# Performance work log

Measured on AMD Instinct MI355X. Metric: run time of the kernel, lower is better.

The kernel has to match this reference:

```python
import jax, jax.numpy as jnp
import numpy as np

DIM = 128
HEADS = 4
DIM_HEAD = 32
HIDDEN = HEADS * DIM_HEAD  # 128
SCALE = DIM_HEAD ** -0.5


def setup_inputs() -> dict:
    key = jax.random.key(0)
    k1, k2, k3, k4 = jax.random.split(key, 4)
    b, c, h, w = 2, DIM, 64, 64
    x = jax.random.normal(k1, (b, c, h, w), dtype=jnp.float32)
    # conv1x1 weights stored as [out_ch, in_ch] (kernel is 1x1)
    w_qkv = jax.random.normal(k2, (3 * HIDDEN, DIM), dtype=jnp.float32) * (DIM ** -0.5)
    w_out = jax.random.normal(k3, (DIM, HIDDEN), dtype=jnp.float32) * (HIDDEN ** -0.5)
    b_out = jax.random.normal(k4, (DIM,), dtype=jnp.float32) * 0.01
    return {"x": x, "w_qkv": w_qkv, "w_out": w_out, "b_out": b_out}


def reference(x, w_qkv, w_out, b_out):
    b, c, h, w = x.shape
    n = h * w
    xf = x.reshape(b, c, n)                                   # [b,c,n]
    qkv = jnp.einsum('oc,bcn->bon', w_qkv, xf)                # conv1x1, no bias
    q, k, v = jnp.split(qkv, 3, axis=1)                       # each [b,hidden,n]
    q = q.reshape(b, HEADS, DIM_HEAD, n) * SCALE
    k = k.reshape(b, HEADS, DIM_HEAD, n)
    v = v.reshape(b, HEADS, DIM_HEAD, n)
    sim = jnp.einsum('bhdi,bhdj->bhij', q, k)                 # [b,h,n,n]
    attn = jax.nn.softmax(sim, axis=-1)
    out = jnp.einsum('bhij,bhdj->bhdi', attn, v)              # [b,h,d,n]
    out = out.reshape(b, HIDDEN, n)
    out = jnp.einsum('oc,bcn->bon', w_out, out) + b_out[None, :, None]
    return out.reshape(b, c, h, w) + x
```

## Files before the change

kernel.cpp:

```cpp
#include <hip/hip_runtime.h>
#include <hip/hip_bf16.h>

typedef __hip_bfloat16 bf16;
typedef float    f32x16 __attribute__((ext_vector_type(16)));
typedef __bf16   bf16x8 __attribute__((ext_vector_type(8)));
typedef unsigned uint4v __attribute__((ext_vector_type(4)));
typedef int      i32x2  __attribute__((ext_vector_type(2)));

#define N_TOK 4096
#define SCALE_L2E 0.2550348952703927f

__device__ __forceinline__ bf16x8 ld8(const bf16* p) { return *(const bf16x8*)p; }
__device__ __forceinline__ unsigned pack2(float a, float b) {
    unsigned short ua = __builtin_bit_cast(unsigned short, (__bf16)a);
    unsigned short ub = __builtin_bit_cast(unsigned short, (__bf16)b);
    return (unsigned)ua | ((unsigned)ub << 16);
}
__device__ __forceinline__ unsigned short f2b(float f) {
    return __builtin_bit_cast(unsigned short, (__bf16)f);
}
__device__ __forceinline__ __bf16 us2bf(unsigned short u) {
    return __builtin_bit_cast(__bf16, u);
}
__device__ __forceinline__ bf16x8 ldw(const unsigned short* rowp) {
    uint2 lo = *(const uint2*)rowp;
    uint2 hi = *(const uint2*)(rowp + 4);
    uint4v u = {lo.x, lo.y, hi.x, hi.y};
    return __builtin_bit_cast(bf16x8, u);
}

__global__ void __launch_bounds__(256)
qkv_mfma(const float* __restrict__ x, const float* __restrict__ w,
         bf16* __restrict__ qt, bf16* __restrict__ kt, bf16* __restrict__ vt) {
    int tok0 = blockIdx.x * 32;
    int b    = blockIdx.y;
    int z    = blockIdx.z;
    __shared__ unsigned short xs[128][32];
    __shared__ unsigned short wl[128][132];
    {
        int c = threadIdx.x >> 1, hf = threadIdx.x & 1;
        const float4* x4 = (const float4*)(x + (size_t)b * (128 * N_TOK) +
                                           (size_t)c * N_TOK + tok0 + hf * 16);
        float4 a = x4[0], bb = x4[1], cc = x4[2], dd = x4[3];
        unsigned* dst = (unsigned*)&xs[c][hf * 16];
        dst[0] = pack2(a.x, a.y);   dst[1] = pack2(a.z, a.w);
        dst[2] = pack2(bb.x, bb.y); dst[3] = pack2(bb.z, bb.w);
        dst[4] = pack2(cc.x, cc.y); dst[5] = pack2(cc.z, cc.w);
        dst[6] = pack2(dd.x, dd.y); dst[7] = pack2(dd.z, dd.w);
    }
    {
        float sc = (z == 0) ? SCALE_L2E : 1.0f;
        const float4* wb4 = (const float4*)(w + (size_t)z * 128 * 128);
#pragma unroll
        for (int s = 0; s < 16; ++s) {
            int i4 = threadIdx.x + s * 256;
            int o  = i4 >> 5, c4 = (i4 & 31) * 4;
            float4 wv4 = wb4[i4];
            *(uint2*)&wl[o][c4] = make_uint2(pack2(wv4.x * sc, wv4.y * sc),
                                             pack2(wv4.z * sc, wv4.w * sc));
        }
    }
    __syncthreads();
    int lane = threadIdx.x & 63, wv = threadIdx.x >> 6;
    int i = lane & 31, hl = lane >> 5;

    bf16x8 xf[8], wf[8];
#pragma unroll
    for (int kb = 0; kb < 8; ++kb) {
        bf16x8 f;
#pragma unroll
        for (int e = 0; e < 8; ++e) f[e] = us2bf(xs[kb * 16 + hl * 8 + e][i]);
        xf[kb] = f;
        wf[kb] = ldw(&wl[wv * 32 + i][kb * 16 + hl * 8]);
    }

    f32x16 D;
#pragma unroll
    for (int r = 0; r < 16; ++r) D[r] = 0.f;

    if (z < 2) {
#pragma unroll
        for (int kb = 0; kb < 8; ++kb)
            D = __builtin_amdgcn_mfma_f32_32x32x16_bf16(xf[kb], wf[kb], D, 0, 0, 0);
        bf16* base = (z == 0) ? qt : kt;
        unsigned short* dst = (unsigned short*)(base + ((size_t)(b * 4 + wv) * N_TOK + tok0) * 32);
#pragma unroll
        for (int r = 0; r < 16; ++r) {
            int tr = (r & 3) + 8 * (r >> 2) + 4 * hl;
            dst[tr * 32 + i] = f2b(D[r]);
        }
    } else {
#pragma unroll
        for (int kb = 0; kb < 8; ++kb)
            D = __builtin_amdgcn_mfma_f32_32x32x16_bf16(wf[kb], xf[kb], D, 0, 0, 0);
        unsigned short* dst = (unsigned short*)(vt + (size_t)(b * 4 + wv) * (32 * N_TOK) + tok0);
#pragma unroll
        for (int r = 0; r < 16; ++r) {
            int dr = (r & 3) + 8 * (r >> 2) + 4 * hl;
            dst[(size_t)dr * N_TOK + i] = f2b(D[r]);
        }
    }
}

__global__ void __launch_bounds__(512)
attn_mfma(const bf16* __restrict__ qt, const bf16* __restrict__ kt,
          const bf16* __restrict__ vt, bf16* __restrict__ ao) {
    int bid   = blockIdx.x;
    int swz   = (bid & 7) * 128 + (bid >> 3);
    int bh    = swz >> 7;
    int qtile = swz & 127;
    int lane  = threadIdx.x & 63;
    int wv    = threadIdx.x >> 6;
    int i     = lane & 31;
    int hl    = lane >> 5;

    const bf16* qb = qt + (size_t)bh * (N_TOK * 32) + (size_t)(qtile * 32) * 32;
    const bf16* kp0 = kt + (size_t)bh * (N_TOK * 32) + ((size_t)(wv * 512) + i) * 32 + hl * 8;
    const bf16* vp0 = vt + (size_t)bh * (32 * N_TOK) + (size_t)i * N_TOK + wv * 512 + hl * 8;

    bf16x8 q1 = ld8(qb + i * 32 + hl * 8);
    bf16x8 q2 = ld8(qb + i * 32 + 16 + hl * 8);

    bf16x8 ones;
#pragma unroll
    for (int e = 0; e < 8; ++e) ones[e] = us2bf(0x3F80);

    f32x16 O, Ol, Z;
#pragma unroll
    for (int r = 0; r < 16; ++r) { O[r] = 0.f; Ol[r] = 0.f; Z[r] = 0.f; }

    bf16x8 kr1[3], kr2[3], vr1[3], vr2[3];
#pragma unroll
    for (int t = 0; t < 3; ++t) {
        kr1[t] = ld8(kp0 + (size_t)(t * 32) * 32);
        kr2[t] = ld8(kp0 + (size_t)(t * 32) * 32 + 16);
        vr1[t] = ld8(vp0 + t * 32);
        vr2[t] = ld8(vp0 + t * 32 + 16);
    }

#pragma unroll
    for (int it = 0; it < 16; ++it) {
        const int cur = it % 3;
        const int jn  = (it * 32 + 96) & 511;

        f32x16 S = __builtin_amdgcn_mfma_f32_32x32x16_bf16(kr1[cur], q1, Z, 0, 0, 0);
        S = __builtin_amdgcn_mfma_f32_32x32x16_bf16(kr2[cur], q2, S, 0, 0, 0);

        kr1[cur] = ld8(kp0 + (size_t)jn * 32);
        kr2[cur] = ld8(kp0 + (size_t)jn * 32 + 16);

        float p[16];
#pragma unroll
        for (int r = 0; r < 16; ++r) p[r] = __builtin_amdgcn_exp2f(S[r]);

        unsigned pk0 = pack2(p[0], p[1]),   pk1 = pack2(p[2], p[3]);
        unsigned pk2 = pack2(p[4], p[5]),   pk3 = pack2(p[6], p[7]);
        unsigned pk4 = pack2(p[8], p[9]),   pk5 = pack2(p[10], p[11]);
        unsigned pk6 = pack2(p[12], p[13]), pk7 = pack2(p[14], p[15]);

        i32x2 s1 = __builtin_amdgcn_permlane32_swap((int)pk0, (int)pk2, false, false);
        i32x2 s2 = __builtin_amdgcn_permlane32_swap((int)pk1, (int)pk3, false, false);
        i32x2 s3 = __builtin_amdgcn_permlane32_swap((int)pk4, (int)pk6, false, false);
        i32x2 s4 = __builtin_amdgcn_permlane32_swap((int)pk5, (int)pk7, false, false);

        uint4v B1u = {(unsigned)s1.x, (unsigned)s2.x, (unsigned)s1.y, (unsigned)s2.y};
        uint4v B2u = {(unsigned)s3.x, (unsigned)s4.x, (unsigned)s3.y, (unsigned)s4.y};
        bf16x8 B1 = __builtin_bit_cast(bf16x8, B1u);
        bf16x8 B2 = __builtin_bit_cast(bf16x8, B2u);

        O  = __builtin_amdgcn_mfma_f32_32x32x16_bf16(vr1[cur], B1, O, 0, 0, 0);
        O  = __builtin_amdgcn_mfma_f32_32x32x16_bf16(vr2[cur], B2, O, 0, 0, 0);
        Ol = __builtin_amdgcn_mfma_f32_32x32x16_bf16(ones, B1, Ol, 0, 0, 0);
        Ol = __builtin_amdgcn_mfma_f32_32x32x16_bf16(ones, B2, Ol, 0, 0, 0);

        vr1[cur] = ld8(vp0 + jn);
        vr2[cur] = ld8(vp0 + jn + 16);
    }

    __shared__ float osh[8][16][64];
    __shared__ float lsh[8][64];
#pragma unroll
    for (int r = 0; r < 16; ++r) osh[wv][r][lane] = O[r];
    lsh[wv][lane] = Ol[0];
    __syncthreads();
    float lt = 0.f;
#pragma unroll
    for (int s = 0; s < 8; ++s) lt += lsh[s][lane];
    float inv = 1.f / lt;
    unsigned short* aop = (unsigned short*)(ao + (size_t)bh * (32 * N_TOK) + qtile * 32);
#pragma unroll
    for (int r = 0; r < 2; ++r) {
        int rr = wv * 2 + r;
        float s = 0.f;
#pragma unroll
        for (int q = 0; q < 8; ++q) s += osh[q][rr][lane];
        int d = (rr & 3) + 8 * (rr >> 2) + 4 * hl;
        aop[(size_t)d * N_TOK + i] = f2b(s * inv);
    }
}

__global__ void __launch_bounds__(256)
out_mfma(const bf16* __restrict__ ao, const float* __restrict__ w,
         const float* __restrict__ bias, const float* __restrict__ x,
         float* __restrict__ out) {
    int tok0 = blockIdx.x * 32;
    int b    = blockIdx.y;
    __shared__ unsigned short as_[128][32];
    __shared__ unsigned short wl[128][132];
    {
        int c = threadIdx.x >> 1, hf = threadIdx.x & 1;
        const uint4v* src = (const uint4v*)(ao + (size_t)b * (128 * N_TOK) +
                                            (size_t)c * N_TOK + tok0 + hf * 16);
        uint4v v0 = src[0], v1 = src[1];
        uint4v* dst = (uint4v*)&as_[c][hf * 16];
        dst[0] = v0; dst[1] = v1;
    }
    {
        const float4* wb4 = (const float4*)w;
#pragma unroll
        for (int s = 0; s < 16; ++s) {
            int i4 = threadIdx.x + s * 256;
            int o  = i4 >> 5, c4 = (i4 & 31) * 4;
            float4 wv4 = wb4[i4];
            *(uint2*)&wl[o][c4] = make_uint2(pack2(wv4.x, wv4.y), pack2(wv4.z, wv4.w));
        }
    }
    __syncthreads();
    int lane = threadIdx.x & 63, wv = threadIdx.x >> 6;
    int i = lane & 31, hl = lane >> 5;

    bf16x8 af[8], wf[8];
#pragma unroll
    for (int kb = 0; kb < 8; ++kb) {
        bf16x8 f;
#pragma unroll
        for (int e = 0; e < 8; ++e) f[e] = us2bf(as_[kb * 16 + hl * 8 + e][i]);
        af[kb] = f;
        wf[kb] = ldw(&wl[wv * 32 + i][kb * 16 + hl * 8]);
    }

    f32x16 D;
#pragma unroll
    for (int r = 0; r < 16; ++r) D[r] = 0.f;
#pragma unroll
    for (int kb = 0; kb < 8; ++kb)
        D = __builtin_amdgcn_mfma_f32_32x32x16_bf16(wf[kb], af[kb], D, 0, 0, 0);

#pragma unroll
    for (int r = 0; r < 16; ++r) {
        int o_r = wv * 32 + (r & 3) + 8 * (r >> 2) + 4 * hl;
        size_t idx = ((size_t)b * 128 + o_r) * N_TOK + tok0 + i;
        out[idx] = D[r] + bias[o_r] + x[idx];
    }
}

extern "C" void kernel_launch(void* const* d_in, const int* in_sizes, int n_in,
                              void* d_out, int out_size, void* d_ws, size_t ws_size,
                              hipStream_t stream) {
    const float* x     = (const float*)d_in[0];
    const float* w_qkv = (const float*)d_in[1];
    const float* w_out = (const float*)d_in[2];
    const float* b_out = (const float*)d_in[3];
    float* out = (float*)d_out;

    bf16* qt = (bf16*)d_ws;
    bf16* kt = qt + (size_t)8 * N_TOK * 32;
    bf16* vt = kt + (size_t)8 * N_TOK * 32;
    bf16* ao = vt + (size_t)8 * N_TOK * 32;

    qkv_mfma <<<dim3(128, 2, 3), 256, 0, stream>>>(x, w_qkv, qt, kt, vt);
    attn_mfma<<<dim3(1024), 512, 0, stream>>>(qt, kt, vt, ao);
    out_mfma <<<dim3(128, 2), 256, 0, stream>>>(ao, w_out, b_out, x, out);
}
```

Measured before the change: 118.6 us.

## Restructure attention kernel to share K/V tiles through double-buffered LDS across query tiles

Each block now handles four 32-query tiles (256 blocks instead of 1024). All waves stream through the full key range in 64-key chunks, and the whole block cooperatively loads each chunk of K and V into double-buffered shared memory. Previously each wave read its own K/V slice from global memory directly for a single query tile. The row sum is now accumulated with scalar adds instead of extra MFMAs against a ones vector, and the cross-wave reduction shrinks to two key halves. The aim is to cut redundant global K/V traffic and MFMA work, at the cost of a __syncthreads per chunk and fewer blocks, which leaves less parallelism across the CUs.

```diff
diff --git a/kernel.cpp b/kernel.cpp
--- a/kernel.cpp
+++ b/kernel.cpp
@@ -105,97 +105,109 @@
 __global__ void __launch_bounds__(512)
 attn_mfma(const bf16* __restrict__ qt, const bf16* __restrict__ kt,
           const bf16* __restrict__ vt, bf16* __restrict__ ao) {
-    int bid   = blockIdx.x;
-    int swz   = (bid & 7) * 128 + (bid >> 3);
-    int bh    = swz >> 7;
-    int qtile = swz & 127;
-    int lane  = threadIdx.x & 63;
-    int wv    = threadIdx.x >> 6;
-    int i     = lane & 31;
-    int hl    = lane >> 5;
-
-    const bf16* qb = qt + (size_t)bh * (N_TOK * 32) + (size_t)(qtile * 32) * 32;
-    const bf16* kp0 = kt + (size_t)bh * (N_TOK * 32) + ((size_t)(wv * 512) + i) * 32 + hl * 8;
-    const bf16* vp0 = vt + (size_t)bh * (32 * N_TOK) + (size_t)i * N_TOK + wv * 512 + hl * 8;
+    int bid = blockIdx.x;
+    int swz = (bid & 7) * 32 + (bid >> 3);
+    int bh  = swz >> 5;
+    int g   = swz & 31;
+    int tid  = threadIdx.x;
+    int lane = tid & 63, wv = tid >> 6;
+    int qtl  = wv >> 1;
+    int kh   = wv & 1;
+    int i    = lane & 31, hl = lane >> 5;
+
+    __shared__ uint4v lds[2][512];
+    __shared__ float  lsh[4][64];
+
+    const bf16* qb = qt + (size_t)bh * (N_TOK * 32) + (size_t)(g * 128 + qtl * 32) * 32;
+    const bf16* kb = kt + (size_t)bh * (N_TOK * 32);
+    const bf16* vb = vt + (size_t)bh * (32 * N_TOK);
 
     bf16x8 q1 = ld8(qb + i * 32 + hl * 8);
     bf16x8 q2 = ld8(qb + i * 32 + 16 + hl * 8);
 
-    bf16x8 ones;
-#pragma unroll
-    for (int e = 0; e < 8; ++e) ones[e] = us2bf(0x3F80);
-
-    f32x16 O, Ol, Z;
-#pragma unroll
-    for (int r = 0; r < 16; ++r) { O[r] = 0.f; Ol[r] = 0.f; Z[r] = 0.f; }
-
-    bf16x8 kr1[3], kr2[3], vr1[3], vr2[3];
-#pragma unroll
-    for (int t = 0; t < 3; ++t) {
-        kr1[t] = ld8(kp0 + (size_t)(t * 32) * 32);
-        kr2[t] = ld8(kp0 + (size_t)(t * 32) * 32 + 16);
-        vr1[t] = ld8(vp0 + t * 32);
-        vr2[t] = ld8(vp0 + t * 32 + 16);
-    }
-
-#pragma unroll
-    for (int it = 0; it < 16; ++it) {
-        const int cur = it % 3;
-        const int jn  = (it * 32 + 96) & 511;
-
-        f32x16 S = __builtin_amdgcn_mfma_f32_32x32x16_bf16(kr1[cur], q1, Z, 0, 0, 0);
-        S = __builtin_amdgcn_mfma_f32_32x32x16_bf16(kr2[cur], q2, S, 0, 0, 0);
-
-        kr1[cur] = ld8(kp0 + (size_t)jn * 32);
-        kr2[cur] = ld8(kp0 + (size_t)jn * 32 + 16);
+    bool isK = tid < 256;
+    int  u   = isK ? tid : tid - 256;
+    int kgoff = (((u >> 7) * 32) + (u & 31)) * 32 + ((u >> 6) & 1) * 16 + ((u >> 5) & 1) * 8;
+    int vgoff = (u >> 3) * N_TOK + (u & 7) * 8;
+    int ldst  = isK ? u : (256 + (u & 7) * 32 + (((u >> 3) + (u & 7)) & 31));
+
+    f32x16 O, Z;
+#pragma unroll
+    for (int r = 0; r < 16; ++r) { O[r] = 0.f; Z[r] = 0.f; }
+    float l = 0.f;
+
+    int kidx1 = kh * 128 + lane;
+    int kidx2 = kh * 128 + 64 + lane;
+    int cc0 = kh * 4 + hl,     vidx1 = 256 + cc0 * 32 + ((i + cc0) & 31);
+    int cc1 = kh * 4 + 2 + hl, vidx2 = 256 + cc1 * 32 + ((i + cc1) & 31);
+
+    lds[0][ldst] = isK ? *(const uint4v*)(kb + kgoff) : *(const uint4v*)(vb + vgoff);
+    __syncthreads();
+
+    for (int c = 0; c < 64; ++c) {
+        int bf = c & 1;
+        uint4v nx;
+        if (c < 63) {
+            int j0 = (c + 1) * 64;
+            nx = isK ? *(const uint4v*)(kb + (size_t)j0 * 32 + kgoff)
+                     : *(const uint4v*)(vb + j0 + vgoff);
+        }
+        const uint4v* L = lds[bf];
+
+        bf16x8 ka1 = __builtin_bit_cast(bf16x8, L[kidx1]);
+        bf16x8 ka2 = __builtin_bit_cast(bf16x8, L[kidx2]);
+        f32x16 S = __builtin_amdgcn_mfma_f32_32x32x16_bf16(ka1, q1, Z, 0, 0, 0);
+        S = __builtin_amdgcn_mfma_f32_32x32x16_bf16(ka2, q2, S, 0, 0, 0);
 
         float p[16];
 #pragma unroll
         for (int r = 0; r < 16; ++r) p[r] = __builtin_amdgcn_exp2f(S[r]);
+        float s0 = (p[0] + p[1]) + (p[2] + p[3]);
+        float s1 = (p[4] + p[5]) + (p[6] + p[7]);
+        float s2 = (p[8] + p[9]) + (p[10] + p[11]);
+        float s3 = (p[12] + p[13]) + (p[14] + p[15]);
+        l += (s0 + s1) + (s2 + s3);
 
         unsigned pk0 = pack2(p[0], p[1]),   pk1 = pack2(p[2], p[3]);
         unsigned pk2 = pack2(p[4], p[5]),   pk3 = pack2(p[6], p[7]);
         unsigned pk4 = pack2(p[8], p[9]),   pk5 = pack2(p[10], p[11]);
         unsigned pk6 = pack2(p[12], p[13]), pk7 = pack2(p[14], p[15]);
 
-        i32x2 s1 = __builtin_amdgcn_permlane32_swap((int)pk0, (int)pk2, false, false);
-        i32x2 s2 = __builtin_amdgcn_permlane32_swap((int)pk1, (int)pk3, false, false);
-        i32x2 s3 = __builtin_amdgcn_permlane32_swap((int)pk4, (int)pk6, false, false);
-        i32x2 s4 = __builtin_amdgcn_permlane32_swap((int)pk5, (int)pk7, false, false);
-
-        uint4v B1u = {(unsigned)s1.x, (unsigned)s2.x, (unsigned)s1.y, (unsigned)s2.y};
-        uint4v B2u = {(unsigned)s3.x, (unsigned)s4.x, (unsigned)s3.y, (unsigned)s4.y};
-        bf16x8 B1 = __builtin_bit_cast(bf16x8, B1u);
-        bf16x8 B2 = __builtin_bit_cast(bf16x8, B2u);
-
-        O  = __builtin_amdgcn_mfma_f32_32x32x16_bf16(vr1[cur], B1, O, 0, 0, 0);
-        O  = __builtin_amdgcn_mfma_f32_32x32x16_bf16(vr2[cur], B2, O, 0, 0, 0);
-        Ol = __builtin_amdgcn_mfma_f32_32x32x16_bf16(ones, B1, Ol, 0, 0, 0);
-        Ol = __builtin_amdgcn_mfma_f32_32x32x16_bf16(ones, B2, Ol, 0, 0, 0);
-
-        vr1[cur] = ld8(vp0 + jn);
-        vr2[cur] = ld8(vp0 + jn + 16);
-    }
-
-    __shared__ float osh[8][16][64];
-    __shared__ float lsh[8][64];
-#pragma unroll
-    for (int r = 0; r < 16; ++r) osh[wv][r][lane] = O[r];
-    lsh[wv][lane] = Ol[0];
-    __syncthreads();
-    float lt = 0.f;
-#pragma unroll
-    for (int s = 0; s < 8; ++s) lt += lsh[s][lane];
-    float inv = 1.f / lt;
-    unsigned short* aop = (unsigned short*)(ao + (size_t)bh * (32 * N_TOK) + qtile * 32);
-#pragma unroll
-    for (int r = 0; r < 2; ++r) {
-        int rr = wv * 2 + r;
-        float s = 0.f;
-#pragma unroll
-        for (int q = 0; q < 8; ++q) s += osh[q][rr][lane];
-        int d = (rr & 3) + 8 * (rr >> 2) + 4 * hl;
-        aop[(size_t)d * N_TOK + i] = f2b(s * inv);
+        i32x2 t1 = __builtin_amdgcn_permlane32_swap((int)pk0, (int)pk2, false, false);
+        i32x2 t2 = __builtin_amdgcn_permlane32_swap((int)pk1, (int)pk3, false, false);
+        i32x2 t3 = __builtin_amdgcn_permlane32_swap((int)pk4, (int)pk6, false, false);
+        i32x2 t4 = __builtin_amdgcn_permlane32_swap((int)pk5, (int)pk7, false, false);
+
+        uint4v B1u = {(unsigned)t1.x, (unsigned)t2.x, (unsigned)t1.y, (unsigned)t2.y};
+        uint4v B2u = {(unsigned)t3.x, (unsigned)t4.x, (unsigned)t3.y, (unsigned)t4.y};
+
+        bf16x8 va1 = __builtin_bit_cast(bf16x8, L[vidx1]);
+        bf16x8 va2 = __builtin_bit_cast(bf16x8, L[vidx2]);
+        O = __builtin_amdgcn_mfma_f32_32x32x16_bf16(va1, __builtin_bit_cast(bf16x8, B1u), O, 0, 0, 0);
+        O = __builtin_amdgcn_mfma_f32_32x32x16_bf16(va2, __builtin_bit_cast(bf16x8, B2u), O, 0, 0, 0);
+
+        if (c < 63) lds[bf ^ 1][ldst] = nx;
+        __syncthreads();
+    }
+
+    l += __shfl_xor(l, 32);
+    float* fb = (float*)lds;
+    if (kh == 1) {
+#pragma unroll
+        for (int r = 0; r < 16; ++r) fb[qtl * 1024 + r * 64 + lane] = O[r];
+        lsh[qtl][lane] = l;
+    }
+    __syncthreads();
+    if (kh == 0) {
+        float lt  = l + lsh[qtl][lane];
+        float inv = 1.f / lt;
+        unsigned short* aop = (unsigned short*)(ao + (size_t)bh * (32 * N_TOK) + g * 128 + qtl * 32);
+#pragma unroll
+        for (int r = 0; r < 16; ++r) {
+            float s = O[r] + fb[qtl * 1024 + r * 64 + lane];
+            int d = (r & 3) + 8 * (r >> 2) + 4 * hl;
+            aop[(size_t)d * N_TOK + i] = f2b(s * inv);
+        }
     }
 }
 
@@ -269,6 +281,6 @@
     bf16* ao = vt + (size_t)8 * N_TOK * 32;
 
     qkv_mfma <<<dim3(128, 2, 3), 256, 0, stream>>>(x, w_qkv, qt, kt, vt);
-    attn_mfma<<<dim3(1024), 512, 0, stream>>>(qt, kt, vt, ao);
+    attn_mfma<<<dim3(256), 512, 0, stream>>>(qt, kt, vt, ao);
     out_mfma <<<dim3(128, 2), 256, 0, stream>>>(ao, w_out, b_out, x, out);
 }
```

New measurement: 112.4 us. -5.2%, faster.
